# Performance work log

Measured on AMD Instinct MI355X. Metric: run time of the kernel, lower is better.

The kernel has to match this reference:

```python
import jax, jax.numpy as jnp
import numpy as np

NA, NM, H, RBF = 50000, 16384, 128, 64
GX, GY, GZ, B = 8, 8, 8, 32  # NM = B * GX*GY*GZ
E_AA, E_AM, E_MA = 800000, 400000, 400000
EPS = 1e-5


def setup_inputs() -> dict:
    key = jax.random.key(0)
    k = jax.random.split(key, 24)
    r = lambda i, s: jax.random.normal(k[i], s, jnp.float32)
    u = lambda i, s: jax.random.uniform(k[i], s, jnp.float32)
    ri = lambda i, s, hi: jax.random.randint(k[i], s, 0, hi, jnp.int32)
    return {
        "a_x": r(0, (NA, H)),
        "m_x": r(1, (NM, H)),
        "a2a_edge_index": ri(2, (2, E_AA), NA),
        "a2m_src": ri(3, (E_AM,), NA), "a2m_dst": ri(4, (E_AM,), NM),
        "m2a_src": ri(5, (E_MA,), NM), "m2a_dst": ri(6, (E_MA,), NA),
        "a2a_edge_weights": u(7, (E_AA,)),
        "a2m_edge_weights": u(8, (E_AM,)),
        "m2a_edge_weights": u(9, (E_MA,)),
        "a2a_edge_attr": r(10, (E_AA, RBF)),
        "a2m_edge_attr": r(11, (E_AM, RBF)),
        "m2a_edge_attr": r(12, (E_MA, RBF)),
        # message-passing params (node proj + RBF edge filter) per branch
        "W_short": r(13, (H, H)) / np.sqrt(H), "We_short": r(14, (RBF, H)) / np.sqrt(RBF),
        "W_a2m": r(15, (H, H)) / np.sqrt(H),  "We_a2m": r(16, (RBF, H)) / np.sqrt(RBF),
        "W_m2a": r(17, (H, H)) / np.sqrt(H),  "We_m2a": r(18, (RBF, H)) / np.sqrt(RBF),
        # long-range Conv3d (kernel 3, SAME padding)
        "conv_k": r(19, (H, H, 3, 3, 3)) / np.sqrt(H * 27), "conv_b": jnp.zeros((H,), jnp.float32),
        # LayerNorm affine params
        "g_short": jnp.ones((H,), jnp.float32), "b_short": jnp.zeros((H,), jnp.float32),
        "g_long": jnp.ones((H,), jnp.float32),  "b_long": jnp.zeros((H,), jnp.float32),
        "g_a2m": jnp.ones((H,), jnp.float32),   "b_a2m": jnp.zeros((H,), jnp.float32),
        "g_m2a": jnp.ones((H,), jnp.float32),   "b_m2a": jnp.zeros((H,), jnp.float32),
    }


def _ln(x, g, b):
    mu = x.mean(-1, keepdims=True)
    var = ((x - mu) ** 2).mean(-1, keepdims=True)
    return (x - mu) * jax.lax.rsqrt(var + EPS) * g + b


def _mp(x, src, dst, ew, ea, W, We, dim_size):
    # continuous-filter message pass: msg_e = (W x_src) * (We rbf_e) * w_e ; scatter-sum
    msg = (x[src] @ W) * (ea @ We) * ew[:, None]  # [E, H]
    return jax.ops.segment_sum(msg, dst, num_segments=dim_size)


def reference(a_x, m_x, a2a_edge_index, a2m_src, a2m_dst, m2a_src, m2a_dst,
              a2a_edge_weights, a2m_edge_weights, m2a_edge_weights,
              a2a_edge_attr, a2m_edge_attr, m2a_edge_attr,
              W_short, We_short, W_a2m, We_a2m, W_m2a, We_m2a,
              conv_k, conv_b,
              g_short, b_short, g_long, b_long, g_a2m, b_a2m, g_m2a, b_m2a):
    delta_a, delta_m = a_x, m_x
    # short-range atom branch
    a = _ln(a_x, g_short, b_short)
    a = _mp(a, a2a_edge_index[0], a2a_edge_index[1], a2a_edge_weights,
            a2a_edge_attr, W_short, We_short, NA)
    # long-range mesh branch: LN -> grid Conv3d (NCDHW) -> flatten back
    m = _ln(m_x, g_long, b_long)
    grid = m.reshape(B, GX, GY, GZ, H).transpose(0, 4, 1, 2, 3)  # [B,H,gx,gy,gz]
    grid = jax.lax.conv_general_dilated(
        grid, conv_k, window_strides=(1, 1, 1), padding='SAME',
        dimension_numbers=('NCDHW', 'OIDHW', 'NCDHW')) + conv_b[None, :, None, None, None]
    m = grid.transpose(0, 2, 3, 4, 1).reshape(-1, H)
    # cross messages with post-LN
    a2m_msg = _ln(_mp(a, a2m_src, a2m_dst, a2m_edge_weights, a2m_edge_attr,
                      W_a2m, We_a2m, NM), g_a2m, b_a2m)
    m2a_msg = _ln(_mp(m, m2a_src, m2a_dst, m2a_edge_weights, m2a_edge_attr,
                      W_m2a, We_m2a, NA), g_m2a, b_m2a)
    return (a + m2a_msg + delta_a, m + a2m_msg + delta_m)
```

## Files before the change

### kernel.cpp

```cpp
#include <hip/hip_runtime.h>
#include <hip/hip_bf16.h>

#define H 128
#define RBF 64

typedef __attribute__((ext_vector_type(8))) short bf16x8;
typedef __attribute__((ext_vector_type(4))) float f32x4;

__device__ inline short f2bf(float f) {
  union { float f; unsigned u; } v; v.f = f;
  const unsigned r = (v.u + 0x7FFFu + ((v.u >> 16) & 1u)) >> 16;
  return (short)r;
}

__global__ __launch_bounds__(128) void ln_rows(const float* __restrict__ X,
                                               const float* __restrict__ g,
                                               const float* __restrict__ bb,
                                               float* __restrict__ Y, int N) {
  __shared__ float sh[4];
  const int row = blockIdx.x;
  const int j = threadIdx.x;
  float x = X[(size_t)row * H + j];
  float s = x, q = x * x;
#pragma unroll
  for (int m = 32; m; m >>= 1) {
    s += __shfl_xor(s, m, 64);
    q += __shfl_xor(q, m, 64);
  }
  if ((j & 63) == 0) { sh[(j >> 6) * 2] = s; sh[(j >> 6) * 2 + 1] = q; }
  __syncthreads();
  s = sh[0] + sh[2];
  q = sh[1] + sh[3];
  const float mu = s * 0.0078125f;
  const float var = q * 0.0078125f - mu * mu;
  const float rs = rsqrtf(var + 1e-5f);
  Y[(size_t)row * H + j] = (x - mu) * rs * g[j] + bb[j];
}

__global__ __launch_bounds__(256) void pack_kt(const float* __restrict__ K,
                                               short* __restrict__ Ktb) {
  const int id = blockIdx.x * 256 + threadIdx.x;
  if (id >= 27 * 4 * 8 * 64) return;
  const int l = id & 63;
  int r = id >> 6;
  const int cb = r & 7; r >>= 3;
  const int kb = r & 3;
  const int tap = r >> 2;
  const int o = cb * 16 + (l & 15);
  const int i0 = kb * 32 + (l >> 4) * 8;
  short* out = Ktb + (size_t)id * 8;
#pragma unroll
  for (int j = 0; j < 8; ++j)
    out[j] = f2bf(K[((size_t)o * H + i0 + j) * 27 + tap]);
}

__global__ __launch_bounds__(256) void pack_we3(
    const float* __restrict__ We0, const float* __restrict__ We1,
    const float* __restrict__ We2, short* __restrict__ Wb0,
    short* __restrict__ Wb1, short* __restrict__ Wb2) {
  const int id = blockIdx.x * 256 + threadIdx.x;
  if (id >= 3072) return;
  const int which = id >> 10;
  const int i = id & 1023;
  const float* We = which == 0 ? We0 : which == 1 ? We1 : We2;
  short* Web = which == 0 ? Wb0 : which == 1 ? Wb1 : Wb2;
  const int f = i >> 6, l = i & 63;
  const int h = f >> 3, c = f & 7;
  const int col = (c << 4) + (l & 15);
  const int k0 = h * 32 + (l >> 4) * 8;
  short* o = Web + (size_t)i * 8;
#pragma unroll
  for (int j = 0; j < 8; ++j) o[j] = f2bf(We[(k0 + j) * H + col]);
}

__global__ __launch_bounds__(256) void pack_w3(
    const float* __restrict__ W0, const float* __restrict__ W1,
    const float* __restrict__ W2, short* __restrict__ Wb0,
    short* __restrict__ Wb1, short* __restrict__ Wb2) {
  const int id = blockIdx.x * 256 + threadIdx.x;
  if (id >= 3 * 2048) return;
  const int which = id >> 11;
  const int i = id & 2047;
  const float* W = which == 0 ? W0 : which == 1 ? W1 : W2;
  short* Wb = which == 0 ? Wb0 : which == 1 ? Wb1 : Wb2;
  const int f = i >> 6, l = i & 63;
  const int kb = f >> 3, cb = f & 7;
  const int col = cb * 16 + (l & 15);
  const int k0 = kb * 32 + (l >> 4) * 8;
  short* o = Wb + (size_t)i * 8;
#pragma unroll
  for (int j = 0; j < 8; ++j) o[j] = f2bf(W[(size_t)(k0 + j) * H + col]);
}

__global__ __launch_bounds__(256) void k_hist3(
    const int* __restrict__ d0, const int* __restrict__ d1,
    const int* __restrict__ d2, int E0, int E1, int E2,
    int* __restrict__ cnt, int off1, int off2) {
  int i = blockIdx.x * 256 + threadIdx.x;
  const int stride = gridDim.x * 256;
  const int ET = E0 + E1 + E2;
  for (; i < ET; i += stride) {
    int d, off;
    if (i < E0) { d = d0[i]; off = 0; }
    else if (i < E0 + E1) { d = d1[i - E0]; off = off1; }
    else { d = d2[i - E0 - E1]; off = off2; }
    atomicAdd(&cnt[off + d], 1);
  }
}

__global__ __launch_bounds__(256) void k_blocksum(const int* __restrict__ cnt,
                                                  int* __restrict__ bsum) {
  __shared__ int sh[256];
  const int t = threadIdx.x;
  sh[t] = cnt[blockIdx.x * 256 + t];
  __syncthreads();
#pragma unroll
  for (int o = 128; o; o >>= 1) {
    if (t < o) sh[t] += sh[t + o];
    __syncthreads();
  }
  if (!t) bsum[blockIdx.x] = sh[0];
}

__global__ __launch_bounds__(512) void k_scan512(const int* __restrict__ bsum,
                                                 int* __restrict__ bpre, int NB) {
  __shared__ int sh[512];
  const int t = threadIdx.x;
  const int v = (t < NB) ? bsum[t] : 0;
  sh[t] = v;
  __syncthreads();
  for (int o = 1; o < 512; o <<= 1) {
    const int u = (t >= o) ? sh[t - o] : 0;
    __syncthreads();
    sh[t] += u;
    __syncthreads();
  }
  if (t < NB) bpre[t] = sh[t] - v;
}

__global__ __launch_bounds__(256) void k_apply3(
    const int* __restrict__ cnt, const int* __restrict__ bpre,
    int* __restrict__ rp0, int* __restrict__ rp1, int* __restrict__ rp2,
    int* __restrict__ cursor, int N0, int N1, int N2, int S1, int S2) {
  __shared__ int sh[256];
  const int b = blockIdx.x;
  const int t = threadIdx.x;
  const int gi = b * 256 + t;
  const int v = cnt[gi];
  sh[t] = v;
  __syncthreads();
  for (int o = 1; o < 256; o <<= 1) {
    const int u = (t >= o) ? sh[t - o] : 0;
    __syncthreads();
    sh[t] += u;
    __syncthreads();
  }
  int sb, N;
  int* rp;
  if (b < S1) { sb = 0; N = N0; rp = rp0; }
  else if (b < S2) { sb = S1; N = N1; rp = rp1; }
  else { sb = S2; N = N2; rp = rp2; }
  const int excl = sh[t] - v + bpre[b] - bpre[sb];
  const int il = (b - sb) * 256 + t;
  if (il <= N) {
    rp[il] = excl;
    if (il < N) cursor[gi] = excl;
  }
}

__global__ __launch_bounds__(256) void k_perm2w(
    const int* __restrict__ dst, const int* __restrict__ src,
    const float* __restrict__ ew, const float* __restrict__ ea, int E,
    int* __restrict__ cursor, int2* __restrict__ sd,
    short* __restrict__ eapfp) {
  const int lane = threadIdx.x & 63;
  const int wid = blockIdx.x * 4 + (threadIdx.x >> 6);
  const int nw = gridDim.x * 4;
  if (blockIdx.x == 0 && threadIdx.x < 16)
    sd[E + threadIdx.x] = make_int2(0, -1);
  const int r = lane >> 2;
  const int c = lane & 3;
  for (int ebase = wid * 16; ebase < E; ebase += nw * 16) {
    const int ecnt = min(16, E - ebase);
    int p = 0;
    float w = 0.f;
    if (lane < ecnt) {
      const int e = ebase + lane;
      const int d = dst[e];
      w = ew[e];
      p = atomicAdd(&cursor[d], 1);
      sd[p] = make_int2(src[e], d);
    }
    const int pr = __shfl(p, r, 64);
    const float wr = __shfl(w, r, 64);
    if (r < ecnt) {
      const float* er = ea + ((size_t)(ebase + r)) * RBF + c * 16;
      const float4 x0 = *(const float4*)(er);
      const float4 x1 = *(const float4*)(er + 4);
      const float4 x2 = *(const float4*)(er + 8);
      const float4 x3 = *(const float4*)(er + 12);
      bf16x8 o0, o1;
      o0[0] = f2bf(x0.x * wr); o0[1] = f2bf(x0.y * wr);
      o0[2] = f2bf(x0.z * wr); o0[3] = f2bf(x0.w * wr);
      o0[4] = f2bf(x1.x * wr); o0[5] = f2bf(x1.y * wr);
      o0[6] = f2bf(x1.z * wr); o0[7] = f2bf(x1.w * wr);
      o1[0] = f2bf(x2.x * wr); o1[1] = f2bf(x2.y * wr);
      o1[2] = f2bf(x2.z * wr); o1[3] = f2bf(x2.w * wr);
      o1[4] = f2bf(x3.x * wr); o1[5] = f2bf(x3.y * wr);
      o1[6] = f2bf(x3.z * wr); o1[7] = f2bf(x3.w * wr);
      short* ob = eapfp + (size_t)pr * RBF + c * 16;
      *(bf16x8*)(ob) = o0;
      *(bf16x8*)(ob + 8) = o1;
    }
  }
}

__global__ __launch_bounds__(256, 2) void proj_mfma(
    const float* __restrict__ X, const short* __restrict__ Wb,
    float* __restrict__ Y, int N) {
  __shared__ short xs[64 * 128];
  const int row0 = blockIdx.x * 64;
  const int t = threadIdx.x;
  const int w = t >> 6, lane = t & 63;
  const int l15 = lane & 15, lg = lane >> 4;

#pragma unroll
  for (int it = 0; it < 4; ++it) {
    const int gidx = it * 256 + t;
    const int r = gidx >> 4;
    const int ch = (gidx & 15) * 8;
    const int row = row0 + r;
    float4 v0 = make_float4(0.f, 0.f, 0.f, 0.f), v1 = v0;
    if (row < N) {
      const float* src = X + (size_t)row * H + ch;
      v0 = *(const float4*)(src);
      v1 = *(const float4*)(src + 4);
    }
    bf16x8 pk;
    pk[0] = f2bf(v0.x); pk[1] = f2bf(v0.y); pk[2] = f2bf(v0.z); pk[3] = f2bf(v0.w);
    pk[4] = f2bf(v1.x); pk[5] = f2bf(v1.y); pk[6] = f2bf(v1.z); pk[7] = f2bf(v1.w);
    const int byte0 = (r * 256 + ch * 2) ^ ((r & 7) << 4);
    *(bf16x8*)((char*)xs + byte0) = pk;
  }
  __syncthreads();

  const int cb0 = 2 * w;
  bf16x8 bw[4][2];
#pragma unroll
  for (int kb = 0; kb < 4; ++kb)
#pragma unroll
    for (int ci = 0; ci < 2; ++ci)
      bw[kb][ci] = *(const bf16x8*)(Wb + (((size_t)kb * 8 + cb0 + ci) * 64 +
                                          lane) * 8);

  f32x4 C[4][2];
#pragma unroll
  for (int mt = 0; mt < 4; ++mt) {
    C[mt][0] = (f32x4){0.f, 0.f, 0.f, 0.f};
    C[mt][1] = (f32x4){0.f, 0.f, 0.f, 0.f};
  }
#pragma unroll
  for (int kb = 0; kb < 4; ++kb) {
#pragma unroll
    for (int mt = 0; mt < 4; ++mt) {
      const int r = mt * 16 + l15;
      const int byte0 = (r * 256 + kb * 64 + lg * 16) ^ ((r & 7) << 4);
      const bf16x8 A = *(const bf16x8*)((const char*)xs + byte0);
      C[mt][0] = __builtin_amdgcn_mfma_f32_16x16x32_bf16(A, bw[kb][0], C[mt][0], 0, 0, 0);
      C[mt][1] = __builtin_amdgcn_mfma_f32_16x16x32_bf16(A, bw[kb][1], C[mt][1], 0, 0, 0);
    }
  }
#pragma unroll
  for (int mt = 0; mt < 4; ++mt)
#pragma unroll
    for (int j = 0; j < 4; ++j) {
      const int row = row0 + mt * 16 + lg * 4 + j;
      if (row < N) {
        float* yp = Y + (size_t)row * H + cb0 * 16 + l15;
        yp[0] = C[mt][0][j];
        yp[16] = C[mt][1][j];
      }
    }
}

template <int NPB, bool FUSE_LN>
__global__ __launch_bounds__(256, 3) void gather_mfma(
    const float* __restrict__ P, const short* __restrict__ Web,
    const short* __restrict__ eapfp, const int2* __restrict__ sd,
    const int* __restrict__ rowptr, int N, const float* __restrict__ base,
    const float* __restrict__ skip, const float* __restrict__ g,
    const float* __restrict__ bb, float* __restrict__ out) {
  constexpr int RSTR = (NPB + 1) * 132;
  constexpr int RPAD = RSTR + ((16 - (RSTR & 31)) & 31);
  __shared__ float acc[4 * RPAD];
  const int t = threadIdx.x;
  const int w = t >> 6, lane = t & 63;
  const int n0 = blockIdx.x * NPB;
  for (int u = t; u < 4 * RPAD; u += 256) acc[u] = 0.f;
  const int rp0 = rowptr[n0];
  const int rp1 = rowptr[min(n0 + NPB, N)];
  __syncthreads();
  const int q0 = rp0 >> 4;
  const int q1 = (rp1 + 15) >> 4;

  const int c0 = 2 * w;
  const bf16x8 bw0 = *(const bf16x8*)(Web + ((size_t)((0 + c0) * 64 + lane)) * 8);
  const bf16x8 bw1 = *(const bf16x8*)(Web + ((size_t)((8 + c0) * 64 + lane)) * 8);
  const bf16x8 bw2 = *(const bf16x8*)(Web + ((size_t)((1 + c0) * 64 + lane)) * 8);
  const bf16x8 bw3 = *(const bf16x8*)(Web + ((size_t)((9 + c0) * 64 + lane)) * 8);

  const int l15 = lane & 15, lg = lane >> 4, rbase = lg * 4;
  const int col0 = c0 * 16 + l15;
  float* const arep = acc + lg * RPAD;

  auto LOAD = [&](int q, bf16x8& A0, bf16x8& A1, int4& sp, int4& dp,
                  float* pv) {
    const short* fb = eapfp + ((size_t)(q * 16 + l15)) * RBF + lg * 8;
    A0 = *(const bf16x8*)(fb);
    A1 = *(const bf16x8*)(fb + 32);
    const int4 sd01 = *(const int4*)(sd + (size_t)(q * 16 + rbase));
    const int4 sd23 = *(const int4*)(sd + (size_t)(q * 16 + rbase + 2));
    sp = make_int4(sd01.x, sd01.z, sd23.x, sd23.z);
    dp = make_int4(sd01.y, sd01.w, sd23.y, sd23.w);
    const float* p0 = P + (size_t)sp.x * H + col0;
    const float* p1 = P + (size_t)sp.y * H + col0;
    const float* p2 = P + (size_t)sp.z * H + col0;
    const float* p3 = P + (size_t)sp.w * H + col0;
    pv[0] = p0[0]; pv[4] = p0[16];
    pv[1] = p1[0]; pv[5] = p1[16];
    pv[2] = p2[0]; pv[6] = p2[16];
    pv[3] = p3[0]; pv[7] = p3[16];
  };
  auto COMP = [&](const bf16x8& A0, const bf16x8& A1, const float* pv,
                  const int4& dp) {
    f32x4 C0 = {0.f, 0.f, 0.f, 0.f};
    C0 = __builtin_amdgcn_mfma_f32_16x16x32_bf16(A0, bw0, C0, 0, 0, 0);
    C0 = __builtin_amdgcn_mfma_f32_16x16x32_bf16(A1, bw1, C0, 0, 0, 0);
    f32x4 C1 = {0.f, 0.f, 0.f, 0.f};
    C1 = __builtin_amdgcn_mfma_f32_16x16x32_bf16(A0, bw2, C1, 0, 0, 0);
    C1 = __builtin_amdgcn_mfma_f32_16x16x32_bf16(A1, bw3, C1, 0, 0, 0);
    const int dls[4] = {dp.x - n0, dp.y - n0, dp.z - n0, dp.w - n0};
    int dl[5];
#pragma unroll
    for (int j = 0; j < 4; ++j)
      dl[j] = ((unsigned)dls[j] < (unsigned)NPB) ? dls[j] : NPB;
    dl[4] = -1;
    float c0v = 0.f, c1v = 0.f;
#pragma unroll
    for (int j = 0; j < 4; ++j) {
      c0v += C0[j] * pv[j];
      c1v += C1[j] * pv[4 + j];
      if (dl[j + 1] != dl[j]) {
        float* a0 = arep + dl[j] * 132 + col0;
        a0[0] += c0v;
        a0[16] += c1v;
        c0v = 0.f;
        c1v = 0.f;
      }
    }
  };

  if (q1 > q0) {
    bf16x8 A0a, A1a, A0b, A1b, A0c, A1c;
    int4 spa, dpa, spb, dpb, spc, dpc;
    float pva[8], pvb[8], pvc[8];
    LOAD(q0, A0a, A1a, spa, dpa, pva);
    if (q0 + 1 < q1) LOAD(q0 + 1, A0b, A1b, spb, dpb, pvb);
    int q = q0;
    while (true) {
      if (q + 2 < q1) LOAD(q + 2, A0c, A1c, spc, dpc, pvc);
      COMP(A0a, A1a, pva, dpa);
      if (++q >= q1) break;
      if (q + 2 < q1) LOAD(q + 2, A0a, A1a, spa, dpa, pva);
      COMP(A0b, A1b, pvb, dpb);
      if (++q >= q1) break;
      if (q + 2 < q1) LOAD(q + 2, A0b, A1b, spb, dpb, pvb);
      COMP(A0c, A1c, pvc, dpc);
      if (++q >= q1) break;
    }
  }
  __syncthreads();

  for (int n = w; n < NPB; n += 4) {
    const int node = n0 + n;
    if (node >= N) break;
    const int rb = n * 132 + lane;
    const float v0 = acc[rb] + acc[RPAD + rb] + acc[2 * RPAD + rb] +
                     acc[3 * RPAD + rb];
    const float v1 = acc[rb + 64] + acc[RPAD + rb + 64] +
                     acc[2 * RPAD + rb + 64] + acc[3 * RPAD + rb + 64];
    const size_t i0 = (size_t)node * H + lane;
    if (FUSE_LN) {
      float s = v0 + v1, q = v0 * v0 + v1 * v1;
#pragma unroll
      for (int m = 32; m; m >>= 1) {
        s += __shfl_xor(s, m, 64);
        q += __shfl_xor(q, m, 64);
      }
      const float mu = s * 0.0078125f;
      const float var = q * 0.0078125f - mu * mu;
      const float rs = rsqrtf(var + 1e-5f);
      out[i0] = base[i0] + (v0 - mu) * rs * g[lane] + bb[lane] + skip[i0];
      out[i0 + 64] =
          base[i0 + 64] + (v1 - mu) * rs * g[lane + 64] + bb[lane + 64] + skip[i0 + 64];
    } else {
      out[i0] = v0;
      out[i0 + 64] = v1;
    }
  }
}

__global__ __launch_bounds__(256, 2) void conv3d_mfma(
    const float* __restrict__ Min, const short* __restrict__ Ktb,
    const float* __restrict__ bias, float* __restrict__ Mout) {
  __shared__ short in_s[193 * 128];
  const int b = blockIdx.x >> 3;
  const int x = blockIdx.x & 7;
  const int t = threadIdx.x;
  const int w = t >> 6, lane = t & 63;
  const int l15 = lane & 15, lg = lane >> 4;

  if (t < 128) in_s[192 * 128 + t] = 0;
#pragma unroll
  for (int it = 0; it < 12; ++it) {
    const int gidx = it * 256 + t;
    const int r = gidx >> 4;
    const int ch = (gidx & 15) * 8;
    const int gx = x + (r >> 6) - 1;
    const int yz = r & 63;
    float4 v0 = make_float4(0.f, 0.f, 0.f, 0.f), v1 = v0;
    if (gx >= 0 && gx < 8) {
      const float* src = Min + ((size_t)((b * 8 + gx) * 64 + yz)) * H + ch;
      v0 = *(const float4*)(src);
      v1 = *(const float4*)(src + 4);
    }
    bf16x8 pk;
    pk[0] = f2bf(v0.x); pk[1] = f2bf(v0.y); pk[2] = f2bf(v0.z); pk[3] = f2bf(v0.w);
    pk[4] = f2bf(v1.x); pk[5] = f2bf(v1.y); pk[6] = f2bf(v1.z); pk[7] = f2bf(v1.w);
    const int byte0 = (r * 256 + ch * 2) ^ ((r & 7) << 4);
    *(bf16x8*)((char*)in_s + byte0) = pk;
  }
  __syncthreads();

  const int cb0 = 2 * w;
  f32x4 C[4][2];
#pragma unroll
  for (int mt = 0; mt < 4; ++mt) {
    C[mt][0] = (f32x4){0.f, 0.f, 0.f, 0.f};
    C[mt][1] = (f32x4){0.f, 0.f, 0.f, 0.f};
  }

  auto BP = [&](int u, int cbi) -> const bf16x8* {
    return (const bf16x8*)(Ktb + (((size_t)u * 8) + cb0 + cbi) * 64 * 8 +
                           (size_t)lane * 8);
  };
  bf16x8 Ba0 = *BP(0, 0), Ba1 = *BP(0, 1);
  for (int u = 0; u < 108; ++u) {
    const int un = min(u + 1, 107);
    const bf16x8 Bn0 = *BP(un, 0);
    const bf16x8 Bn1 = *BP(un, 1);
    const int tap = u >> 2, kb = u & 3;
    const int dx = tap / 9, dy = (tap / 3) % 3, dz = tap % 3;
#pragma unroll
    for (int mt = 0; mt < 4; ++mt) {
      const int v = mt * 16 + l15;
      const int y = v >> 3, z = v & 7;
      const int ny = y + dy - 1, nz = z + dz - 1;
      const bool ok = (ny >= 0 && ny < 8 && nz >= 0 && nz < 8);
      const int vrow = ok ? dx * 64 + ny * 8 + nz : 192;
      const int byte0 = ((vrow * 256 + kb * 64 + lg * 16) ^ ((vrow & 7) << 4));
      const bf16x8 A = *(const bf16x8*)((const char*)in_s + byte0);
      C[mt][0] = __builtin_amdgcn_mfma_f32_16x16x32_bf16(A, Ba0, C[mt][0], 0, 0, 0);
      C[mt][1] = __builtin_amdgcn_mfma_f32_16x16x32_bf16(A, Ba1, C[mt][1], 0, 0, 0);
    }
    Ba0 = Bn0;
    Ba1 = Bn1;
  }

  const float b0 = bias[cb0 * 16 + l15];
  const float b1 = bias[cb0 * 16 + 16 + l15];
  float* obase = Mout + ((size_t)((b * 8 + x) * 64)) * H;
#pragma unroll
  for (int mt = 0; mt < 4; ++mt)
#pragma unroll
    for (int j = 0; j < 4; ++j) {
      const int vox = mt * 16 + lg * 4 + j;
      float* op = obase + (size_t)vox * H + cb0 * 16 + l15;
      op[0] = C[mt][0][j] + b0;
      op[16] = C[mt][1][j] + b1;
    }
}

extern "C" void kernel_launch(void* const* d_in, const int* in_sizes, int n_in,
                              void* d_out, int out_size, void* d_ws, size_t ws_size,
                              hipStream_t stream) {
  const float* a_x = (const float*)d_in[0];
  const float* m_x = (const float*)d_in[1];
  const int* aa_idx = (const int*)d_in[2];
  const int* a2m_src = (const int*)d_in[3];
  const int* a2m_dst = (const int*)d_in[4];
  const int* m2a_src = (const int*)d_in[5];
  const int* m2a_dst = (const int*)d_in[6];
  const float* aa_w = (const float*)d_in[7];
  const float* a2m_w = (const float*)d_in[8];
  const float* m2a_w = (const float*)d_in[9];
  const float* aa_ea = (const float*)d_in[10];
  const float* a2m_ea = (const float*)d_in[11];
  const float* m2a_ea = (const float*)d_in[12];
  const float* W_short = (const float*)d_in[13];
  const float* We_short = (const float*)d_in[14];
  const float* W_a2m = (const float*)d_in[15];
  const float* We_a2m = (const float*)d_in[16];
  const float* W_m2a = (const float*)d_in[17];
  const float* We_m2a = (const float*)d_in[18];
  const float* conv_k = (const float*)d_in[19];
  const float* conv_b = (const float*)d_in[20];
  const float* g_short = (const float*)d_in[21];
  const float* b_short = (const float*)d_in[22];
  const float* g_long = (const float*)d_in[23];
  const float* b_long = (const float*)d_in[24];
  const float* g_a2m = (const float*)d_in[25];
  const float* b_a2m = (const float*)d_in[26];
  const float* g_m2a = (const float*)d_in[27];
  const float* b_m2a = (const float*)d_in[28];

  const int NA = in_sizes[0] / H;
  const int NM = in_sizes[1] / H;
  const int E_AA = in_sizes[2] / 2;
  const int E_AM = in_sizes[3];
  const int E_MA = in_sizes[5];
  const int* aa_src = aa_idx;
  const int* aa_dst = aa_idx + E_AA;

  const int NB_A = (NA + 256) / 256;
  const int NB_M = (NM + 256) / 256;
  const int S1 = NB_A, S2 = NB_A + NB_M;
  const int NB_T = NB_A + NB_M + NB_A;
  const int OFF1 = S1 * 256, OFF2 = S2 * 256;

  float* ws = (float*)d_ws;
  float* p_buf = ws;
  float* m1_buf = p_buf + (size_t)NA * H;
  float* m2_buf = m1_buf + (size_t)NM * H;
  float* a2_buf = m2_buf + (size_t)NM * H;
  float* a1_buf = a2_buf + (size_t)NA * H;
  short* web_aa = (short*)(a1_buf + (size_t)NA * H);
  short* web_a2m = web_aa + 8192;
  short* web_m2a = web_a2m + 8192;
  short* wb_s = web_m2a + 8192;
  short* wb_a2m = wb_s + 16384;
  short* wb_m2a = wb_a2m + 16384;
  short* ktb = wb_m2a + 16384;
  short* eapfp = ktb + 442368;
  int2* sd_aa = (int2*)(eapfp + (size_t)E_AA * RBF);
  int2* sd_a2m = sd_aa + E_AA + 16;
  int2* sd_m2a = sd_a2m + E_AM + 16;
  int* iws = (int*)(sd_m2a + E_MA + 16);
  int* cnt = iws;       iws += NB_T * 256;
  int* cursor = iws;    iws += NB_T * 256;
  int* bsum = iws;      iws += 512;
  int* bpre = iws;      iws += 512;
  int* rp_aa = iws;     iws += NA + 1;
  int* rp_a2m = iws;    iws += NM + 1;
  int* rp_m2a = iws;    iws += NA + 1;

  float* out_a = (float*)d_out;
  float* out_m = out_a + (size_t)NA * H;

  pack_we3<<<12, 256, 0, stream>>>(We_short, We_a2m, We_m2a, web_aa, web_a2m,
                                   web_m2a);
  pack_w3<<<24, 256, 0, stream>>>(W_short, W_a2m, W_m2a, wb_s, wb_a2m, wb_m2a);
  pack_kt<<<(27 * 4 * 8 * 64 + 255) / 256, 256, 0, stream>>>(conv_k, ktb);
  ln_rows<<<NM, 128, 0, stream>>>(m_x, g_long, b_long, m1_buf, NM);
  conv3d_mfma<<<(NM / 64), 256, 0, stream>>>(m1_buf, ktb, conv_b, m2_buf);
  ln_rows<<<NA, 128, 0, stream>>>(a_x, g_short, b_short, a1_buf, NA);
  proj_mfma<<<(NA + 63) / 64, 256, 0, stream>>>(a1_buf, wb_s, p_buf, NA);

  hipMemsetAsync(cnt, 0, (size_t)NB_T * 256 * sizeof(int), stream);
  k_hist3<<<2048, 256, 0, stream>>>(aa_dst, a2m_dst, m2a_dst, E_AA, E_AM, E_MA,
                                    cnt, OFF1, OFF2);
  k_blocksum<<<NB_T, 256, 0, stream>>>(cnt, bsum);
  k_scan512<<<1, 512, 0, stream>>>(bsum, bpre, NB_T);
  k_apply3<<<NB_T, 256, 0, stream>>>(cnt, bpre, rp_aa, rp_a2m, rp_m2a, cursor,
                                     NA, NM, NA, S1, S2);

  k_perm2w<<<2048, 256, 0, stream>>>(aa_dst, aa_src, aa_w, aa_ea, E_AA, cursor,
                                     sd_aa, eapfp);
  gather_mfma<16, false><<<(NA + 15) / 16, 256, 0, stream>>>(
      p_buf, web_aa, eapfp, sd_aa, rp_aa, NA, nullptr, nullptr, nullptr,
      nullptr, a2_buf);

  proj_mfma<<<(NA + 63) / 64, 256, 0, stream>>>(a2_buf, wb_a2m, p_buf, NA);
  k_perm2w<<<2048, 256, 0, stream>>>(a2m_dst, a2m_src, a2m_w, a2m_ea, E_AM,
                                     cursor + OFF1, sd_a2m, eapfp);
  gather_mfma<16, true><<<(NM + 15) / 16, 256, 0, stream>>>(
      p_buf, web_a2m, eapfp, sd_a2m, rp_a2m, NM, m2_buf, m_x, g_a2m, b_a2m,
      out_m);

  proj_mfma<<<(NM + 63) / 64, 256, 0, stream>>>(m2_buf, wb_m2a, m1_buf, NM);
  k_perm2w<<<2048, 256, 0, stream>>>(m2a_dst, m2a_src, m2a_w, m2a_ea, E_MA,
                                     cursor + OFF2, sd_m2a, eapfp);
  gather_mfma<16, true><<<(NA + 15) / 16, 256, 0, stream>>>(
      m1_buf, web_m2a, eapfp, sd_m2a, rp_m2a, NA, a2_buf, a_x, g_m2a, b_m2a,
      out_a);
}
```

Measured before the change: 557.7 us.

## Drop permuted bf16 edge-attr copy; gather fp32 edge attrs by index in gather kernel

The permutation kernel no longer rewrites edge attributes into a dst-sorted bf16 buffer. It now writes only a (src, dst, edge id, weight) record per edge, and all three edge sets are permuted in a single launch. The gather kernel reads the original fp32 edge attributes through the edge id, converts them to bf16 in registers, and applies the edge weight after the MFMA instead of before. This avoids writing and re-reading a large intermediate buffer, but replaces contiguous 128-byte bf16 reads with random 256-byte fp32 reads in the gather, and the prefetch depth drops from three stages to two.

```diff
diff --git a/kernel.cpp b/kernel.cpp
--- a/kernel.cpp
+++ b/kernel.cpp
@@ -168,50 +168,33 @@
   }
 }
 
-__global__ __launch_bounds__(256) void k_perm2w(
-    const int* __restrict__ dst, const int* __restrict__ src,
-    const float* __restrict__ ew, const float* __restrict__ ea, int E,
-    int* __restrict__ cursor, int2* __restrict__ sd,
-    short* __restrict__ eapfp) {
-  const int lane = threadIdx.x & 63;
-  const int wid = blockIdx.x * 4 + (threadIdx.x >> 6);
-  const int nw = gridDim.x * 4;
-  if (blockIdx.x == 0 && threadIdx.x < 16)
-    sd[E + threadIdx.x] = make_int2(0, -1);
-  const int r = lane >> 2;
-  const int c = lane & 3;
-  for (int ebase = wid * 16; ebase < E; ebase += nw * 16) {
-    const int ecnt = min(16, E - ebase);
-    int p = 0;
-    float w = 0.f;
-    if (lane < ecnt) {
-      const int e = ebase + lane;
-      const int d = dst[e];
-      w = ew[e];
-      p = atomicAdd(&cursor[d], 1);
-      sd[p] = make_int2(src[e], d);
-    }
-    const int pr = __shfl(p, r, 64);
-    const float wr = __shfl(w, r, 64);
-    if (r < ecnt) {
-      const float* er = ea + ((size_t)(ebase + r)) * RBF + c * 16;
-      const float4 x0 = *(const float4*)(er);
-      const float4 x1 = *(const float4*)(er + 4);
-      const float4 x2 = *(const float4*)(er + 8);
-      const float4 x3 = *(const float4*)(er + 12);
-      bf16x8 o0, o1;
-      o0[0] = f2bf(x0.x * wr); o0[1] = f2bf(x0.y * wr);
-      o0[2] = f2bf(x0.z * wr); o0[3] = f2bf(x0.w * wr);
-      o0[4] = f2bf(x1.x * wr); o0[5] = f2bf(x1.y * wr);
-      o0[6] = f2bf(x1.z * wr); o0[7] = f2bf(x1.w * wr);
-      o1[0] = f2bf(x2.x * wr); o1[1] = f2bf(x2.y * wr);
-      o1[2] = f2bf(x2.z * wr); o1[3] = f2bf(x2.w * wr);
-      o1[4] = f2bf(x3.x * wr); o1[5] = f2bf(x3.y * wr);
-      o1[6] = f2bf(x3.z * wr); o1[7] = f2bf(x3.w * wr);
-      short* ob = eapfp + (size_t)pr * RBF + c * 16;
-      *(bf16x8*)(ob) = o0;
-      *(bf16x8*)(ob + 8) = o1;
-    }
+__global__ __launch_bounds__(256) void k_perm3x(
+    const int* __restrict__ d0, const int* __restrict__ s0,
+    const float* __restrict__ w0, const int* __restrict__ d1,
+    const int* __restrict__ s1, const float* __restrict__ w1,
+    const int* __restrict__ d2, const int* __restrict__ s2,
+    const float* __restrict__ w2, int E0, int E1, int E2,
+    int* __restrict__ cursor, int off1, int off2, int4* __restrict__ sde0,
+    int4* __restrict__ sde1, int4* __restrict__ sde2) {
+  if (blockIdx.x == 0 && threadIdx.x < 48) {
+    const int wsel = threadIdx.x >> 4;
+    const int j = threadIdx.x & 15;
+    int4* sp = wsel == 0 ? sde0 + E0 : wsel == 1 ? sde1 + E1 : sde2 + E2;
+    sp[j] = make_int4(0, -1, 0, 0);
+  }
+  int i = blockIdx.x * 256 + threadIdx.x;
+  const int stride = gridDim.x * 256;
+  const int ET = E0 + E1 + E2;
+  for (; i < ET; i += stride) {
+    int e, d, s;
+    float w;
+    int* cur;
+    int4* sde;
+    if (i < E0) { e = i; d = d0[e]; s = s0[e]; w = w0[e]; cur = cursor; sde = sde0; }
+    else if (i < E0 + E1) { e = i - E0; d = d1[e]; s = s1[e]; w = w1[e]; cur = cursor + off1; sde = sde1; }
+    else { e = i - E0 - E1; d = d2[e]; s = s2[e]; w = w2[e]; cur = cursor + off2; sde = sde2; }
+    const int p = atomicAdd(&cur[d], 1);
+    sde[p] = make_int4(s, d, e, __float_as_int(w));
   }
 }
 
@@ -286,7 +269,7 @@
 template <int NPB, bool FUSE_LN>
 __global__ __launch_bounds__(256, 3) void gather_mfma(
     const float* __restrict__ P, const short* __restrict__ Web,
-    const short* __restrict__ eapfp, const int2* __restrict__ sd,
+    const float* __restrict__ ea, const int4* __restrict__ sde,
     const int* __restrict__ rowptr, int N, const float* __restrict__ base,
     const float* __restrict__ skip, const float* __restrict__ g,
     const float* __restrict__ bb, float* __restrict__ out) {
@@ -313,15 +296,26 @@
   const int col0 = c0 * 16 + l15;
   float* const arep = acc + lg * RPAD;
 
-  auto LOAD = [&](int q, bf16x8& A0, bf16x8& A1, int4& sp, int4& dp,
-                  float* pv) {
-    const short* fb = eapfp + ((size_t)(q * 16 + l15)) * RBF + lg * 8;
-    A0 = *(const bf16x8*)(fb);
-    A1 = *(const bf16x8*)(fb + 32);
-    const int4 sd01 = *(const int4*)(sd + (size_t)(q * 16 + rbase));
-    const int4 sd23 = *(const int4*)(sd + (size_t)(q * 16 + rbase + 2));
-    sp = make_int4(sd01.x, sd01.z, sd23.x, sd23.z);
-    dp = make_int4(sd01.y, sd01.w, sd23.y, sd23.w);
+  auto ISSUE = [&](int q, float4& e0, float4& e1, float4& e2, float4& e3,
+                   int4& sp, int4& dp, float4& wq, float* pv) {
+    const int4 r4 = sde[(size_t)(q * 16 + l15)];
+    const float* er = ea + (size_t)r4.z * RBF + lg * 8;
+    e0 = *(const float4*)(er);
+    e1 = *(const float4*)(er + 4);
+    e2 = *(const float4*)(er + 32);
+    e3 = *(const float4*)(er + 36);
+    const float wf = __int_as_float(r4.w);
+    int sj[4], dj[4];
+    float wj[4];
+#pragma unroll
+    for (int j = 0; j < 4; ++j) {
+      sj[j] = __shfl(r4.x, rbase + j, 16);
+      dj[j] = __shfl(r4.y, rbase + j, 16);
+      wj[j] = __shfl(wf, rbase + j, 16);
+    }
+    sp = make_int4(sj[0], sj[1], sj[2], sj[3]);
+    dp = make_int4(dj[0], dj[1], dj[2], dj[3]);
+    wq = make_float4(wj[0], wj[1], wj[2], wj[3]);
     const float* p0 = P + (size_t)sp.x * H + col0;
     const float* p1 = P + (size_t)sp.y * H + col0;
     const float* p2 = P + (size_t)sp.z * H + col0;
@@ -331,14 +325,21 @@
     pv[2] = p2[0]; pv[6] = p2[16];
     pv[3] = p3[0]; pv[7] = p3[16];
   };
-  auto COMP = [&](const bf16x8& A0, const bf16x8& A1, const float* pv,
-                  const int4& dp) {
+  auto COMP = [&](const float4& e0, const float4& e1, const float4& e2,
+                  const float4& e3, const float* pv, const int4& dp,
+                  const float4& wq) {
+    bf16x8 A0, A1;
+    A0[0] = f2bf(e0.x); A0[1] = f2bf(e0.y); A0[2] = f2bf(e0.z); A0[3] = f2bf(e0.w);
+    A0[4] = f2bf(e1.x); A0[5] = f2bf(e1.y); A0[6] = f2bf(e1.z); A0[7] = f2bf(e1.w);
+    A1[0] = f2bf(e2.x); A1[1] = f2bf(e2.y); A1[2] = f2bf(e2.z); A1[3] = f2bf(e2.w);
+    A1[4] = f2bf(e3.x); A1[5] = f2bf(e3.y); A1[6] = f2bf(e3.z); A1[7] = f2bf(e3.w);
     f32x4 C0 = {0.f, 0.f, 0.f, 0.f};
     C0 = __builtin_amdgcn_mfma_f32_16x16x32_bf16(A0, bw0, C0, 0, 0, 0);
     C0 = __builtin_amdgcn_mfma_f32_16x16x32_bf16(A1, bw1, C0, 0, 0, 0);
     f32x4 C1 = {0.f, 0.f, 0.f, 0.f};
     C1 = __builtin_amdgcn_mfma_f32_16x16x32_bf16(A0, bw2, C1, 0, 0, 0);
     C1 = __builtin_amdgcn_mfma_f32_16x16x32_bf16(A1, bw3, C1, 0, 0, 0);
+    const float wqa[4] = {wq.x, wq.y, wq.z, wq.w};
     const int dls[4] = {dp.x - n0, dp.y - n0, dp.z - n0, dp.w - n0};
     int dl[5];
 #pragma unroll
@@ -348,8 +349,8 @@
     float c0v = 0.f, c1v = 0.f;
 #pragma unroll
     for (int j = 0; j < 4; ++j) {
-      c0v += C0[j] * pv[j];
-      c1v += C1[j] * pv[4 + j];
+      c0v += C0[j] * pv[j] * wqa[j];
+      c1v += C1[j] * pv[4 + j] * wqa[j];
       if (dl[j + 1] != dl[j]) {
         float* a0 = arep + dl[j] * 132 + col0;
         a0[0] += c0v;
@@ -361,22 +362,19 @@
   };
 
   if (q1 > q0) {
-    bf16x8 A0a, A1a, A0b, A1b, A0c, A1c;
-    int4 spa, dpa, spb, dpb, spc, dpc;
-    float pva[8], pvb[8], pvc[8];
-    LOAD(q0, A0a, A1a, spa, dpa, pva);
-    if (q0 + 1 < q1) LOAD(q0 + 1, A0b, A1b, spb, dpb, pvb);
-    int q = q0;
-    while (true) {
-      if (q + 2 < q1) LOAD(q + 2, A0c, A1c, spc, dpc, pvc);
-      COMP(A0a, A1a, pva, dpa);
-      if (++q >= q1) break;
-      if (q + 2 < q1) LOAD(q + 2, A0a, A1a, spa, dpa, pva);
-      COMP(A0b, A1b, pvb, dpb);
-      if (++q >= q1) break;
-      if (q + 2 < q1) LOAD(q + 2, A0b, A1b, spb, dpb, pvb);
-      COMP(A0c, A1c, pvc, dpc);
-      if (++q >= q1) break;
+    float4 eA0, eA1, eA2, eA3, eB0, eB1, eB2, eB3;
+    int4 spA, dpA, spB, dpB;
+    float4 wqA, wqB;
+    float pvA[8], pvB[8];
+    ISSUE(q0, eA0, eA1, eA2, eA3, spA, dpA, wqA, pvA);
+    if (q0 + 1 < q1) ISSUE(q0 + 1, eB0, eB1, eB2, eB3, spB, dpB, wqB, pvB);
+    for (int q = q0; q < q1; q += 2) {
+      COMP(eA0, eA1, eA2, eA3, pvA, dpA, wqA);
+      if (q + 2 < q1) ISSUE(q + 2, eA0, eA1, eA2, eA3, spA, dpA, wqA, pvA);
+      if (q + 1 < q1) {
+        COMP(eB0, eB1, eB2, eB3, pvB, dpB, wqB);
+        if (q + 3 < q1) ISSUE(q + 3, eB0, eB1, eB2, eB3, spB, dpB, wqB, pvB);
+      }
     }
   }
   __syncthreads();
@@ -551,11 +549,10 @@
   short* wb_a2m = wb_s + 16384;
   short* wb_m2a = wb_a2m + 16384;
   short* ktb = wb_m2a + 16384;
-  short* eapfp = ktb + 442368;
-  int2* sd_aa = (int2*)(eapfp + (size_t)E_AA * RBF);
-  int2* sd_a2m = sd_aa + E_AA + 16;
-  int2* sd_m2a = sd_a2m + E_AM + 16;
-  int* iws = (int*)(sd_m2a + E_MA + 16);
+  int4* sde_aa = (int4*)(ktb + 442368);
+  int4* sde_a2m = sde_aa + E_AA + 16;
+  int4* sde_m2a = sde_a2m + E_AM + 16;
+  int* iws = (int*)(sde_m2a + E_MA + 16);
   int* cnt = iws;       iws += NB_T * 256;
   int* cursor = iws;    iws += NB_T * 256;
   int* bsum = iws;      iws += 512;
@@ -583,24 +580,22 @@
   k_scan512<<<1, 512, 0, stream>>>(bsum, bpre, NB_T);
   k_apply3<<<NB_T, 256, 0, stream>>>(cnt, bpre, rp_aa, rp_a2m, rp_m2a, cursor,
                                      NA, NM, NA, S1, S2);
-
-  k_perm2w<<<2048, 256, 0, stream>>>(aa_dst, aa_src, aa_w, aa_ea, E_AA, cursor,
-                                     sd_aa, eapfp);
+  k_perm3x<<<2048, 256, 0, stream>>>(aa_dst, aa_src, aa_w, a2m_dst, a2m_src,
+                                     a2m_w, m2a_dst, m2a_src, m2a_w, E_AA,
+                                     E_AM, E_MA, cursor, OFF1, OFF2, sde_aa,
+                                     sde_a2m, sde_m2a);
+
   gather_mfma<16, false><<<(NA + 15) / 16, 256, 0, stream>>>(
-      p_buf, web_aa, eapfp, sd_aa, rp_aa, NA, nullptr, nullptr, nullptr,
+      p_buf, web_aa, aa_ea, sde_aa, rp_aa, NA, nullptr, nullptr, nullptr,
       nullptr, a2_buf);
 
   proj_mfma<<<(NA + 63) / 64, 256, 0, stream>>>(a2_buf, wb_a2m, p_buf, NA);
-  k_perm2w<<<2048, 256, 0, stream>>>(a2m_dst, a2m_src, a2m_w, a2m_ea, E_AM,
-                                     cursor + OFF1, sd_a2m, eapfp);
   gather_mfma<16, true><<<(NM + 15) / 16, 256, 0, stream>>>(
-      p_buf, web_a2m, eapfp, sd_a2m, rp_a2m, NM, m2_buf, m_x, g_a2m, b_a2m,
+      p_buf, web_a2m, a2m_ea, sde_a2m, rp_a2m, NM, m2_buf, m_x, g_a2m, b_a2m,
       out_m);
 
   proj_mfma<<<(NM + 63) / 64, 256, 0, stream>>>(m2_buf, wb_m2a, m1_buf, NM);
-  k_perm2w<<<2048, 256, 0, stream>>>(m2a_dst, m2a_src, m2a_w, m2a_ea, E_MA,
-                                     cursor + OFF2, sd_m2a, eapfp);
   gather_mfma<16, true><<<(NA + 15) / 16, 256, 0, stream>>>(
-      m1_buf, web_m2a, eapfp, sd_m2a, rp_m2a, NA, a2_buf, a_x, g_m2a, b_m2a,
+      m1_buf, web_m2a, m2a_ea, sde_m2a, rp_m2a, NA, a2_buf, a_x, g_m2a, b_m2a,
       out_a);
 }
```

After: 621.1 us. 11.4% more time.
